# Kernel optimization log

Measured on AMD Instinct MI355X. Metric: run time of the kernel, lower is better.

Reference implementation:

```python
import jax, jax.numpy as jnp
import numpy as np

D_MODEL = 1024
D_FF = 4096
NUM_EXPERTS = 8
TOP_K = 2  # expert_capacity


def setup_inputs() -> dict:
    key = jax.random.key(0)
    ks = jax.random.split(key, 7)
    s_in = 1.0 / np.sqrt(D_MODEL)
    s_ff = 1.0 / np.sqrt(D_FF)
    x = jax.random.normal(ks[0], (2, 2048, D_MODEL), dtype=jnp.float32)
    gate_w = jax.random.uniform(ks[1], (NUM_EXPERTS, D_MODEL), jnp.float32, -s_in, s_in)
    gate_b = jax.random.uniform(ks[2], (NUM_EXPERTS,), jnp.float32, -s_in, s_in)
    w1 = jax.random.uniform(ks[3], (NUM_EXPERTS, D_MODEL, D_FF), jnp.float32, -s_in, s_in)
    b1 = jax.random.uniform(ks[4], (NUM_EXPERTS, D_FF), jnp.float32, -s_in, s_in)
    w2 = jax.random.uniform(ks[5], (NUM_EXPERTS, D_FF, D_MODEL), jnp.float32, -s_ff, s_ff)
    b2 = jax.random.uniform(ks[6], (NUM_EXPERTS, D_MODEL), jnp.float32, -s_ff, s_ff)
    return {"x": x, "gate_w": gate_w, "gate_b": gate_b,
            "w1": w1, "b1": b1, "w2": w2, "b2": b2}


def reference(x, gate_w, gate_b, w1, b1, w2, b2):
    E = gate_w.shape[0]
    # Router
    logits = jnp.einsum('bsd,ed->bse', x, gate_w) + gate_b  # [B,S,E]
    top_vals, top_idx = jax.lax.top_k(logits, TOP_K)        # [B,S,K]
    top_w = jax.nn.softmax(top_vals, axis=-1)               # softmax over the top-k logits
    probs = jax.nn.softmax(logits, axis=-1)
    usage = probs.mean(axis=(0, 1))                         # [E]
    load_balancing_loss = E * jnp.sum(usage ** 2) - 1.0
    # Combine weights: sum over top-k slots of weight * one_hot(expert)
    combine = jnp.sum(top_w[..., None] * jax.nn.one_hot(top_idx, E, dtype=x.dtype), axis=2)  # [B,S,E]
    # All experts over all tokens (faithful to the naive dense-then-mask module)
    h = jax.nn.gelu(jnp.einsum('bsd,edf->ebsf', x, w1) + b1[:, None, None, :], approximate=False)
    expert_out = jnp.einsum('ebsf,efd->ebsd', h, w2) + b2[:, None, None, :]  # [E,B,S,D]
    output = jnp.einsum('bse,ebsd->bsd', combine, expert_out)
    return output, load_balancing_loss
```

## Files before the change

### kernel.cpp

```cpp
#include <hip/hip_runtime.h>
#include <hip/hip_bf16.h>
#include <math.h>


#define D_MODEL 1024
#define D_FF    4096
#define NE      8
#define NTOK    4096
#define CAP     4096

typedef __attribute__((ext_vector_type(4))) float f32x4;
typedef __attribute__((ext_vector_type(4))) short s16x4;
typedef __attribute__((ext_vector_type(8))) short s16x8;

__device__ __forceinline__ short f2bf(float f) {
    union { float f; unsigned u; } v; v.f = f;
    unsigned r = v.u + 0x7FFFu + ((v.u >> 16) & 1u);
    return (short)(r >> 16);
}

__device__ __forceinline__ float gelu_f(float x) {
    float u = x * x;
    float v = __builtin_fmaf(0.044715f, u, 1.0f);
    float y2 = 1.5957691216057308f * x * v;
    float r = __builtin_amdgcn_rcpf(__expf(y2) + 1.0f);
    return x - x * r;
}

__device__ __forceinline__ void gload16(const void* g, void* l) {
    __builtin_amdgcn_global_load_lds(
        (const __attribute__((address_space(1))) unsigned*)g,
        (__attribute__((address_space(3))) unsigned*)l, 16, 0, 0);
}

__global__ __launch_bounds__(256) void router_kernel(
    const float* __restrict__ x, const float* __restrict__ gw,
    const float* __restrict__ gb,
    float* __restrict__ usage, int* __restrict__ eidx, float* __restrict__ wgt,
    short* __restrict__ xb)
{
    __shared__ float s_gw[NE][D_MODEL];
    __shared__ float s_usage[NE];
    int tid = threadIdx.x;
    for (int i = tid * 4; i < NE * D_MODEL; i += 256 * 4)
        *(f32x4*)&s_gw[0][i] = *(const f32x4*)(gw + i);
    if (tid < NE) s_usage[tid] = 0.f;
    __syncthreads();

    int wid = tid >> 6, lane = tid & 63;
    int wave_stride = gridDim.x * 4;
    float l_usage[NE];
#pragma unroll
    for (int e = 0; e < NE; e++) l_usage[e] = 0.f;

    for (int t = blockIdx.x * 4 + wid; t < NTOK; t += wave_stride) {
        const float* xr = x + (size_t)t * D_MODEL;
        short* xbr = xb + (size_t)t * D_MODEL;
        float acc[NE];
#pragma unroll
        for (int e = 0; e < NE; e++) acc[e] = 0.f;
        for (int i = lane * 4; i < D_MODEL; i += 64 * 4) {
            f32x4 xv = *(const f32x4*)(xr + i);
            s16x4 bv;
#pragma unroll
            for (int j = 0; j < 4; j++) bv[j] = f2bf(xv[j]);
            *(s16x4*)(xbr + i) = bv;
#pragma unroll
            for (int e = 0; e < NE; e++) {
                f32x4 gv = *(const f32x4*)&s_gw[e][i];
                acc[e] += xv[0]*gv[0] + xv[1]*gv[1] + xv[2]*gv[2] + xv[3]*gv[3];
            }
        }
#pragma unroll
        for (int e = 0; e < NE; e++) {
            float a = acc[e];
            for (int off = 32; off; off >>= 1) a += __shfl_down(a, off);
            acc[e] = a;
        }
        if (lane == 0) {
            float logits[NE];
            float mx = -1e30f;
#pragma unroll
            for (int e = 0; e < NE; e++) { logits[e] = acc[e] + gb[e]; mx = fmaxf(mx, logits[e]); }
            float se = 0.f;
            float pe[NE];
#pragma unroll
            for (int e = 0; e < NE; e++) { pe[e] = expf(logits[e] - mx); se += pe[e]; }
            float inv = 1.f / se;
#pragma unroll
            for (int e = 0; e < NE; e++) l_usage[e] += pe[e] * inv;
            int i0 = 0;
#pragma unroll
            for (int e = 1; e < NE; e++) if (logits[e] > logits[i0]) i0 = e;
            int i1 = -1;
#pragma unroll
            for (int e = 0; e < NE; e++) {
                if (e == i0) continue;
                if (i1 < 0 || logits[e] > logits[i1]) i1 = e;
            }
            float w0 = 1.f / (1.f + expf(logits[i1] - logits[i0]));
            eidx[t] = i0 | (i1 << 8);
            wgt[t] = w0;
        }
    }
    if (lane == 0) {
#pragma unroll
        for (int e = 0; e < NE; e++) atomicAdd(&s_usage[e], l_usage[e]);
    }
    __syncthreads();
    if (tid < NE) atomicAdd(&usage[tid], s_usage[tid]);
}

__global__ __launch_bounds__(256) void build_lists(
    const int* __restrict__ eidx, const float* __restrict__ wgt,
    int* __restrict__ cnt, int* __restrict__ tok_list, float* __restrict__ wt_list,
    int* __restrict__ tok2slot, float* __restrict__ wgt_p)
{
    int e = blockIdx.x;
    __shared__ int s_cnt;
    if (threadIdx.x == 0) s_cnt = 0;
    __syncthreads();
    for (int t = threadIdx.x; t < NTOK; t += 256) {
        int p = eidx[t];
        float w0 = wgt[t];
        if (e == 0) wgt_p[t] = w0;
        if ((p & 255) == e) {
            int s = atomicAdd(&s_cnt, 1);
            tok_list[e * CAP + s] = t; wt_list[e * CAP + s] = w0;
            tok2slot[2 * t] = (e << 16) | s;
        }
        if ((p >> 8) == e) {
            int s = atomicAdd(&s_cnt, 1);
            tok_list[e * CAP + s] = t; wt_list[e * CAP + s] = 1.f - w0;
            tok2slot[2 * t + 1] = (e << 16) | s;
        }
    }
    __syncthreads();
    if (threadIdx.x == 0) cnt[e] = s_cnt;
}

__global__ void compute_offsets(const int* __restrict__ cnt, int* __restrict__ offsets)
{
    int o = 0;
    for (int e = 0; e < NE; e++) { offsets[e] = o; o += cnt[e]; }
}

__global__ void write_loss(const float* __restrict__ usage, float* __restrict__ out_loss)
{
    float s = 0.f;
    for (int e = 0; e < NE; e++) { float u = usage[e] / (float)NTOK; s += u * u; }
    *out_loss = (float)NE * s - 1.f;
}

__global__ __launch_bounds__(256) void transpose_cvt(
    const float* __restrict__ src, short* __restrict__ dst, int R, int C)
{
    __shared__ float tile[64][65];
    int e = blockIdx.z;
    src += (size_t)e * R * C;
    dst += (size_t)e * R * C;
    int c0 = blockIdx.x * 64, r0 = blockIdx.y * 64;
    int tid = threadIdx.x;
    int lr = tid >> 2, lc = (tid & 3) * 16;

    const float* s = src + (size_t)(r0 + lr) * C + c0 + lc;
#pragma unroll
    for (int j = 0; j < 4; j++)
        *(f32x4*)&tile[lr][lc + j * 4] = *(const f32x4*)(s + j * 4);
    __syncthreads();

    short* d = dst + (size_t)(c0 + lr) * R + r0 + lc;
    s16x8 v0, v1;
#pragma unroll
    for (int j = 0; j < 8; j++) v0[j] = f2bf(tile[lc + j][lr]);
#pragma unroll
    for (int j = 0; j < 8; j++) v1[j] = f2bf(tile[lc + 8 + j][lr]);
    *(s16x8*)d = v0;
    *(s16x8*)(d + 8) = v1;
}

#define GEMM_STAGE(AS, BS, KT)                       \
    gload16(asrc0 + (KT), &AS[wid * 16][0]);         \
    gload16(asrc1 + (KT), &AS[64 + wid * 16][0]);    \
    gload16(bsrc0 + (KT), &BS[wid * 16][0]);         \
    gload16(bsrc1 + (KT), &BS[64 + wid * 16][0]);

#define GEMM_COMPUTE(AS, BS)                                                   \
    {                                                                          \
        s16x8 a[4], b[4];                                                      \
        int cidx = (kgr ^ ((lrow >> 1) & 3)) * 8;                              \
        _Pragma("unroll")                                                      \
        for (int i = 0; i < 4; i++) {                                          \
            a[i] = *(const s16x8*)&AS[wr * 64 + i * 16 + lrow][cidx];          \
            b[i] = *(const s16x8*)&BS[wc * 64 + i * 16 + lrow][cidx];          \
        }                                                                      \
        _Pragma("unroll")                                                      \
        for (int i = 0; i < 4; i++)                                            \
            _Pragma("unroll")                                                  \
            for (int j = 0; j < 4; j++)                                        \
                acc[i][j] = __builtin_amdgcn_mfma_f32_16x16x32_bf16(           \
                    a[i], b[j], acc[i][j], 0, 0, 0);                           \
    }

__global__ __launch_bounds__(256) void gemm1_kernel(
    const short* __restrict__ XB, const short* __restrict__ W1T,
    const float* __restrict__ b1, const int* __restrict__ cnt,
    const int* __restrict__ offsets, const int* __restrict__ tok_list,
    short* __restrict__ H)
{
    int r = blockIdx.x;
    int s = (r & 7) * 1024 + (r >> 3);
    int bx = s & 31;
    int by = s >> 5;
    int e  = by >> 5;
    int tm = by & 31;
    int ce = cnt[e];
    if (tm * 128 >= ce) return;
    int n0 = bx * 128;

    __shared__ __align__(16) short As[128][32];
    __shared__ __align__(16) short Bs[128][32];

    int tid = threadIdx.x;
    int lane = tid & 63, wid = tid >> 6;
    int wr = wid >> 1, wc = wid & 1;
    int lrow = lane & 15, kgr = lane >> 4;

    int srow = wid * 16 + (lane >> 2);
    int scol = ((lane & 3) ^ ((lane >> 3) & 3)) * 8;
    int am0 = tm * 128 + srow, am1 = am0 + 64;
    int tok0 = tok_list[e * CAP + (am0 < ce ? am0 : 0)];
    int tok1 = tok_list[e * CAP + (am1 < ce ? am1 : 0)];
    const short* asrc0 = XB + (size_t)tok0 * D_MODEL + scol;
    const short* asrc1 = XB + (size_t)tok1 * D_MODEL + scol;
    const short* bsrc0 = W1T + ((size_t)e * D_FF + n0 + srow) * D_MODEL + scol;
    const short* bsrc1 = bsrc0 + (size_t)64 * D_MODEL;

    f32x4 acc[4][4] = {};
    for (int kt = 0; kt < D_MODEL; kt += 32) {
        GEMM_STAGE(As, Bs, kt);
        __syncthreads();
        GEMM_COMPUTE(As, Bs);
        __syncthreads();
    }

    int offe = offsets[e];
    float bn[4];
#pragma unroll
    for (int j = 0; j < 4; j++) bn[j] = b1[e * D_FF + n0 + wc * 64 + j * 16 + lrow];
#pragma unroll
    for (int i = 0; i < 4; i++) {
#pragma unroll
        for (int q = 0; q < 4; q++) {
            int m = tm * 128 + wr * 64 + i * 16 + kgr * 4 + q;
            if (m >= ce) continue;
            short* hrow = H + (size_t)(offe + m) * D_FF;
#pragma unroll
            for (int j = 0; j < 4; j++) {
                int n = n0 + wc * 64 + j * 16 + lrow;
                hrow[n] = f2bf(gelu_f(acc[i][j][q] + bn[j]));
            }
        }
    }
}

__global__ __launch_bounds__(256) void gemm2_y_kernel(
    const short* __restrict__ H, const short* __restrict__ W2T,
    const float* __restrict__ b2, const int* __restrict__ cnt,
    const int* __restrict__ offsets, float* __restrict__ Y)
{
    int r = blockIdx.x;
    int s = (r & 7) * 256 + (r >> 3);
    int bx = s & 7;
    int by = s >> 3;
    int e  = by >> 5;
    int tm = by & 31;
    int ce = cnt[e];
    if (tm * 128 >= ce) return;
    int offe = offsets[e];
    int n0 = bx * 128;

    __shared__ __align__(16) short As[128][32];
    __shared__ __align__(16) short Bs[128][32];

    int tid = threadIdx.x;
    int lane = tid & 63, wid = tid >> 6;
    int wr = wid >> 1, wc = wid & 1;
    int lrow = lane & 15, kgr = lane >> 4;

    int srow = wid * 16 + (lane >> 2);
    int scol = ((lane & 3) ^ ((lane >> 3) & 3)) * 8;
    int am0 = tm * 128 + srow, am1 = am0 + 64;
    const short* asrc0 = H + (size_t)(offe + (am0 < ce ? am0 : 0)) * D_FF + scol;
    const short* asrc1 = H + (size_t)(offe + (am1 < ce ? am1 : 0)) * D_FF + scol;
    const short* bsrc0 = W2T + ((size_t)e * D_MODEL + n0 + srow) * D_FF + scol;
    const short* bsrc1 = bsrc0 + (size_t)64 * D_FF;

    f32x4 acc[4][4] = {};
    for (int kt = 0; kt < D_FF; kt += 32) {
        GEMM_STAGE(As, Bs, kt);
        __syncthreads();
        GEMM_COMPUTE(As, Bs);
        __syncthreads();
    }

    float bn[4];
#pragma unroll
    for (int j = 0; j < 4; j++) bn[j] = b2[e * D_MODEL + n0 + wc * 64 + j * 16 + lrow];
#pragma unroll
    for (int i = 0; i < 4; i++) {
#pragma unroll
        for (int q = 0; q < 4; q++) {
            int m = tm * 128 + wr * 64 + i * 16 + kgr * 4 + q;
            if (m >= ce) continue;
            float* yrow = Y + (size_t)(offe + m) * D_MODEL;
#pragma unroll
            for (int j = 0; j < 4; j++) {
                int n = n0 + wc * 64 + j * 16 + lrow;
                yrow[n] = acc[i][j][q] + bn[j];
            }
        }
    }
}

__global__ __launch_bounds__(256) void combine_kernel(
    const float* __restrict__ Y, const int* __restrict__ tok2slot,
    const float* __restrict__ wgt_p, const int* __restrict__ offsets,
    float* __restrict__ out)
{
    int t = blockIdx.x;
    int d = threadIdx.x * 4;
    int p0 = tok2slot[2 * t], p1 = tok2slot[2 * t + 1];
    int s0 = offsets[p0 >> 16] + (p0 & 0xFFFF);
    int s1 = offsets[p1 >> 16] + (p1 & 0xFFFF);
    float w0 = wgt_p[t], w1 = 1.f - w0;
    f32x4 a = *(const f32x4*)(Y + (size_t)s0 * D_MODEL + d);
    f32x4 b = *(const f32x4*)(Y + (size_t)s1 * D_MODEL + d);
    f32x4 r;
#pragma unroll
    for (int j = 0; j < 4; j++) r[j] = w0 * a[j] + w1 * b[j];
    *(f32x4*)(out + (size_t)t * D_MODEL + d) = r;
}

__global__ __launch_bounds__(256) void gemm2_kernel(
    const short* __restrict__ H, const short* __restrict__ W2T,
    const float* __restrict__ b2, const int* __restrict__ cnt,
    const int* __restrict__ offsets, const int* __restrict__ tok_list,
    const float* __restrict__ wt_list, float* __restrict__ out)
{
    int e  = blockIdx.y >> 5;
    int tm = blockIdx.y & 31;
    int ce = cnt[e];
    if (tm * 128 >= ce) return;
    int offe = offsets[e];
    int n0 = blockIdx.x * 128;
    int kz = blockIdx.z;
    const int KSPAN = D_FF / 2;
    int kbase = kz * KSPAN;

    __shared__ __align__(16) short As[128][32];
    __shared__ __align__(16) short Bs[128][32];

    int tid = threadIdx.x;
    int lane = tid & 63, wid = tid >> 6;
    int wr = wid >> 1, wc = wid & 1;
    int lrow = lane & 15, kgr = lane >> 4;

    int srow = wid * 16 + (lane >> 2);
    int scol = ((lane & 3) ^ ((lane >> 3) & 3)) * 8;
    int am0 = tm * 128 + srow, am1 = am0 + 64;
    const short* asrc0 = H + (size_t)(offe + (am0 < ce ? am0 : 0)) * D_FF + kbase + scol;
    const short* asrc1 = H + (size_t)(offe + (am1 < ce ? am1 : 0)) * D_FF + kbase + scol;
    const short* bsrc0 = W2T + ((size_t)e * D_MODEL + n0 + srow) * D_FF + kbase + scol;
    const short* bsrc1 = bsrc0 + (size_t)64 * D_FF;

    f32x4 acc[4][4] = {};
    for (int kt = 0; kt < KSPAN; kt += 32) {
        GEMM_STAGE(As, Bs, kt);
        __syncthreads();
        GEMM_COMPUTE(As, Bs);
        __syncthreads();
    }

    float bn[4];
#pragma unroll
    for (int j = 0; j < 4; j++)
        bn[j] = (kz == 0) ? b2[e * D_MODEL + n0 + wc * 64 + j * 16 + lrow] : 0.f;
#pragma unroll
    for (int i = 0; i < 4; i++) {
#pragma unroll
        for (int q = 0; q < 4; q++) {
            int m = tm * 128 + wr * 64 + i * 16 + kgr * 4 + q;
            if (m >= ce) continue;
            int tokm = tok_list[e * CAP + m];
            float wt = wt_list[e * CAP + m];
            float* orow = out + (size_t)tokm * D_MODEL;
#pragma unroll
            for (int j = 0; j < 4; j++) {
                int n = n0 + wc * 64 + j * 16 + lrow;
                atomicAdd(&orow[n], wt * (acc[i][j][q] + bn[j]));
            }
        }
    }
}

extern "C" void kernel_launch(void* const* d_in, const int* in_sizes, int n_in,
                              void* d_out, int out_size, void* d_ws, size_t ws_size,
                              hipStream_t stream)
{
    const float* x  = (const float*)d_in[0];
    const float* gw = (const float*)d_in[1];
    const float* gb = (const float*)d_in[2];
    const float* w1 = (const float*)d_in[3];
    const float* b1 = (const float*)d_in[4];
    const float* w2 = (const float*)d_in[5];
    const float* b2 = (const float*)d_in[6];
    float* out = (float*)d_out;

    char* w = (char*)d_ws;
    int*   cnt      = (int*)(w + 0);
    float* usage    = (float*)(w + 32);
    int*   offsets  = (int*)(w + 64);
    int*   tok_list = (int*)(w + 128);
    float* wt_list  = (float*)(w + 128 + 131072);
    int*   tok2slot = (int*)(w + 128 + 262144);
    float* wgt_p    = (float*)(w + 128 + 262144 + 32768);
    short* WT       = (short*)(w + 311424);
    short* H        = (short*)(w + 311424 + 67108864ull);
    float* Y        = (float*)(w + 311424 + 2ull * 67108864ull);
    size_t need_y   = 311424 + 2ull * 67108864ull + 33554432ull;
    bool   use_y    = ws_size >= need_y;
    int*   eidx     = (int*)WT;
    float* wgt      = (float*)(WT + NTOK * 2);
    short* XB       = (short*)d_out;

    hipMemsetAsync(d_ws, 0, 128, stream);

    router_kernel<<<256, 256, 0, stream>>>(x, gw, gb, usage, eidx, wgt, XB);
    build_lists<<<NE, 256, 0, stream>>>(eidx, wgt, cnt, tok_list, wt_list, tok2slot, wgt_p);
    compute_offsets<<<1, 1, 0, stream>>>(cnt, offsets);

    transpose_cvt<<<dim3(D_FF / 64, D_MODEL / 64, NE), 256, 0, stream>>>(w1, WT, D_MODEL, D_FF);
    gemm1_kernel<<<(D_FF / 128) * NE * (CAP / 128), 256, 0, stream>>>(
        XB, WT, b1, cnt, offsets, tok_list, H);

    transpose_cvt<<<dim3(D_MODEL / 64, D_FF / 64, NE), 256, 0, stream>>>(w2, WT, D_FF, D_MODEL);

    if (use_y) {
        write_loss<<<1, 1, 0, stream>>>(usage, out + (size_t)NTOK * D_MODEL);
        gemm2_y_kernel<<<2048, 256, 0, stream>>>(H, WT, b2, cnt, offsets, Y);
        combine_kernel<<<NTOK, 256, 0, stream>>>(Y, tok2slot, wgt_p, offsets, out);
    } else {
        hipMemsetAsync(d_out, 0, (size_t)out_size * sizeof(float), stream);
        write_loss<<<1, 1, 0, stream>>>(usage, out + (size_t)NTOK * D_MODEL);
        gemm2_kernel<<<dim3(D_MODEL / 128, NE * (CAP / 128), 2), 256, 0, stream>>>(
            H, WT, b2, cnt, offsets, tok_list, wt_list, out);
    }
}
```

Baseline: 348.1 us.

## Merge router and both weight transposes into one prep kernel; fold offsets/loss into build_lists

When the workspace is large enough, the router and the bf16 transposes of w1 and w2 now run as block ranges of one kernel, with separate W1T and W2T buffers. This removes several launches and lets the weight conversions overlap with routing. build_lists also computes offsets and the loss in its last block, found through an atomic counter, which drops two tiny serial launches. In exchange it needs an extra 64MB of workspace, and the prep kernel's shared-memory union is sized for the router, which can lower occupancy for the transpose blocks.

```diff
diff --git a/kernel.cpp b/kernel.cpp
--- a/kernel.cpp
+++ b/kernel.cpp
@@ -33,27 +33,28 @@
         (__attribute__((address_space(3))) unsigned*)l, 16, 0, 0);
 }
 
-__global__ __launch_bounds__(256) void router_kernel(
+
+struct RouterSmem { float gw[NE][D_MODEL]; float us[NE]; };
+
+__device__ void router_body(
     const float* __restrict__ x, const float* __restrict__ gw,
-    const float* __restrict__ gb,
-    float* __restrict__ usage, int* __restrict__ eidx, float* __restrict__ wgt,
-    short* __restrict__ xb)
-{
-    __shared__ float s_gw[NE][D_MODEL];
-    __shared__ float s_usage[NE];
+    const float* __restrict__ gb, float* __restrict__ usage,
+    int* __restrict__ eidx, float* __restrict__ wgt, short* __restrict__ xb,
+    RouterSmem* sm, int rb, int nblk)
+{
     int tid = threadIdx.x;
     for (int i = tid * 4; i < NE * D_MODEL; i += 256 * 4)
-        *(f32x4*)&s_gw[0][i] = *(const f32x4*)(gw + i);
-    if (tid < NE) s_usage[tid] = 0.f;
+        *(f32x4*)&sm->gw[0][i] = *(const f32x4*)(gw + i);
+    if (tid < NE) sm->us[tid] = 0.f;
     __syncthreads();
 
     int wid = tid >> 6, lane = tid & 63;
-    int wave_stride = gridDim.x * 4;
+    int wave_stride = nblk * 4;
     float l_usage[NE];
 #pragma unroll
     for (int e = 0; e < NE; e++) l_usage[e] = 0.f;
 
-    for (int t = blockIdx.x * 4 + wid; t < NTOK; t += wave_stride) {
+    for (int t = rb * 4 + wid; t < NTOK; t += wave_stride) {
         const float* xr = x + (size_t)t * D_MODEL;
         short* xbr = xb + (size_t)t * D_MODEL;
         float acc[NE];
@@ -67,7 +68,7 @@
             *(s16x4*)(xbr + i) = bv;
 #pragma unroll
             for (int e = 0; e < NE; e++) {
-                f32x4 gv = *(const f32x4*)&s_gw[e][i];
+                f32x4 gv = *(const f32x4*)&sm->gw[e][i];
                 acc[e] += xv[0]*gv[0] + xv[1]*gv[1] + xv[2]*gv[2] + xv[3]*gv[3];
             }
         }
@@ -105,16 +106,80 @@
     }
     if (lane == 0) {
 #pragma unroll
-        for (int e = 0; e < NE; e++) atomicAdd(&s_usage[e], l_usage[e]);
+        for (int e = 0; e < NE; e++) atomicAdd(&sm->us[e], l_usage[e]);
     }
     __syncthreads();
-    if (tid < NE) atomicAdd(&usage[tid], s_usage[tid]);
+    if (tid < NE) atomicAdd(&usage[tid], sm->us[tid]);
+}
+
+__device__ void transpose_body(
+    const float* __restrict__ src, short* __restrict__ dst, int R, int C,
+    int bx, int by, int e, float (*tile)[65])
+{
+    src += (size_t)e * R * C;
+    dst += (size_t)e * R * C;
+    int c0 = bx * 64, r0 = by * 64;
+    int tid = threadIdx.x;
+    int lr = tid >> 2, lc = (tid & 3) * 16;
+
+    const float* s = src + (size_t)(r0 + lr) * C + c0 + lc;
+#pragma unroll
+    for (int j = 0; j < 4; j++)
+        *(f32x4*)&tile[lr][lc + j * 4] = *(const f32x4*)(s + j * 4);
+    __syncthreads();
+
+    short* d = dst + (size_t)(c0 + lr) * R + r0 + lc;
+    s16x8 v0, v1;
+#pragma unroll
+    for (int j = 0; j < 8; j++) v0[j] = f2bf(tile[lc + j][lr]);
+#pragma unroll
+    for (int j = 0; j < 8; j++) v1[j] = f2bf(tile[lc + 8 + j][lr]);
+    *(s16x8*)d = v0;
+    *(s16x8*)(d + 8) = v1;
+}
+
+__global__ __launch_bounds__(256) void prep_kernel(
+    const float* __restrict__ x, const float* __restrict__ gw,
+    const float* __restrict__ gb, float* __restrict__ usage,
+    int* __restrict__ eidx, float* __restrict__ wgt, short* __restrict__ xb,
+    const float* __restrict__ w1, short* __restrict__ w1t,
+    const float* __restrict__ w2, short* __restrict__ w2t)
+{
+    __shared__ union { RouterSmem r; float tile[64][65]; } sm;
+    int b = blockIdx.x;
+    if (b < 256) {
+        router_body(x, gw, gb, usage, eidx, wgt, xb, &sm.r, b, 256);
+    } else if (b < 256 + 8192) {
+        int q = b - 256;
+        transpose_body(w1, w1t, D_MODEL, D_FF, q & 63, (q >> 6) & 15, q >> 10, sm.tile);
+    } else {
+        int q = b - 256 - 8192;
+        transpose_body(w2, w2t, D_FF, D_MODEL, q & 15, (q >> 4) & 63, q >> 10, sm.tile);
+    }
+}
+
+__global__ __launch_bounds__(256) void router_kernel(
+    const float* __restrict__ x, const float* __restrict__ gw,
+    const float* __restrict__ gb, float* __restrict__ usage,
+    int* __restrict__ eidx, float* __restrict__ wgt, short* __restrict__ xb)
+{
+    __shared__ RouterSmem sm;
+    router_body(x, gw, gb, usage, eidx, wgt, xb, &sm, blockIdx.x, gridDim.x);
+}
+
+__global__ __launch_bounds__(256) void transpose_cvt(
+    const float* __restrict__ src, short* __restrict__ dst, int R, int C)
+{
+    __shared__ float tile[64][65];
+    transpose_body(src, dst, R, C, blockIdx.x, blockIdx.y, blockIdx.z, tile);
 }
 
 __global__ __launch_bounds__(256) void build_lists(
     const int* __restrict__ eidx, const float* __restrict__ wgt,
     int* __restrict__ cnt, int* __restrict__ tok_list, float* __restrict__ wt_list,
-    int* __restrict__ tok2slot, float* __restrict__ wgt_p)
+    int* __restrict__ tok2slot, float* __restrict__ wgt_p,
+    int* __restrict__ done, int* __restrict__ offsets,
+    const float* __restrict__ usage, float* __restrict__ out_loss)
 {
     int e = blockIdx.x;
     __shared__ int s_cnt;
@@ -136,13 +201,20 @@
         }
     }
     __syncthreads();
-    if (threadIdx.x == 0) cnt[e] = s_cnt;
-}
-
-__global__ void compute_offsets(const int* __restrict__ cnt, int* __restrict__ offsets)
-{
-    int o = 0;
-    for (int e = 0; e < NE; e++) { offsets[e] = o; o += cnt[e]; }
+    if (threadIdx.x == 0) {
+        cnt[e] = s_cnt;
+        __threadfence();
+        if (atomicAdd(done, 1) == NE - 1) {
+            __threadfence();
+            int o = 0;
+            for (int k = 0; k < NE; k++) { offsets[k] = o; o += cnt[k]; }
+            if (out_loss) {
+                float s = 0.f;
+                for (int k = 0; k < NE; k++) { float u = usage[k] / (float)NTOK; s += u * u; }
+                *out_loss = (float)NE * s - 1.f;
+            }
+        }
+    }
 }
 
 __global__ void write_loss(const float* __restrict__ usage, float* __restrict__ out_loss)
@@ -150,33 +222,6 @@
     float s = 0.f;
     for (int e = 0; e < NE; e++) { float u = usage[e] / (float)NTOK; s += u * u; }
     *out_loss = (float)NE * s - 1.f;
-}
-
-__global__ __launch_bounds__(256) void transpose_cvt(
-    const float* __restrict__ src, short* __restrict__ dst, int R, int C)
-{
-    __shared__ float tile[64][65];
-    int e = blockIdx.z;
-    src += (size_t)e * R * C;
-    dst += (size_t)e * R * C;
-    int c0 = blockIdx.x * 64, r0 = blockIdx.y * 64;
-    int tid = threadIdx.x;
-    int lr = tid >> 2, lc = (tid & 3) * 16;
-
-    const float* s = src + (size_t)(r0 + lr) * C + c0 + lc;
-#pragma unroll
-    for (int j = 0; j < 4; j++)
-        *(f32x4*)&tile[lr][lc + j * 4] = *(const f32x4*)(s + j * 4);
-    __syncthreads();
-
-    short* d = dst + (size_t)(c0 + lr) * R + r0 + lc;
-    s16x8 v0, v1;
-#pragma unroll
-    for (int j = 0; j < 8; j++) v0[j] = f2bf(tile[lc + j][lr]);
-#pragma unroll
-    for (int j = 0; j < 8; j++) v1[j] = f2bf(tile[lc + 8 + j][lr]);
-    *(s16x8*)d = v0;
-    *(s16x8*)(d + 8) = v1;
 }
 
 #define GEMM_STAGE(AS, BS, KT)                       \
@@ -421,38 +466,63 @@
     int*   cnt      = (int*)(w + 0);
     float* usage    = (float*)(w + 32);
     int*   offsets  = (int*)(w + 64);
+    int*   done     = (int*)(w + 96);
     int*   tok_list = (int*)(w + 128);
     float* wt_list  = (float*)(w + 128 + 131072);
     int*   tok2slot = (int*)(w + 128 + 262144);
     float* wgt_p    = (float*)(w + 128 + 262144 + 32768);
-    short* WT       = (short*)(w + 311424);
-    short* H        = (short*)(w + 311424 + 67108864ull);
-    float* Y        = (float*)(w + 311424 + 2ull * 67108864ull);
-    size_t need_y   = 311424 + 2ull * 67108864ull + 33554432ull;
-    bool   use_y    = ws_size >= need_y;
-    int*   eidx     = (int*)WT;
-    float* wgt      = (float*)(WT + NTOK * 2);
+    const size_t MB64 = 67108864ull;
     short* XB       = (short*)d_out;
-
+    float* out_loss = out + (size_t)NTOK * D_MODEL;
+
+    size_t need_sep = 311424 + 3ull * MB64;
+    size_t need_y1  = 311424 + 2ull * MB64 + 33554432ull;
     hipMemsetAsync(d_ws, 0, 128, stream);
 
+    if (ws_size >= need_sep) {
+        short* W1T = (short*)(w + 311424);
+        short* W2T = (short*)(w + 311424 + MB64);
+        short* H   = (short*)(w + 311424 + 2 * MB64);
+        float* Y   = (float*)W1T;
+        int*   eidx = (int*)H;
+        float* wgt  = (float*)((char*)H + 16384);
+
+        prep_kernel<<<256 + 8192 + 8192, 256, 0, stream>>>(
+            x, gw, gb, usage, eidx, wgt, XB, w1, W1T, w2, W2T);
+        build_lists<<<NE, 256, 0, stream>>>(
+            eidx, wgt, cnt, tok_list, wt_list, tok2slot, wgt_p,
+            done, offsets, usage, out_loss);
+        gemm1_kernel<<<(D_FF / 128) * NE * (CAP / 128), 256, 0, stream>>>(
+            XB, W1T, b1, cnt, offsets, tok_list, H);
+        gemm2_y_kernel<<<2048, 256, 0, stream>>>(H, W2T, b2, cnt, offsets, Y);
+        combine_kernel<<<NTOK, 256, 0, stream>>>(Y, tok2slot, wgt_p, offsets, out);
+        return;
+    }
+
+    short* WT  = (short*)(w + 311424);
+    short* H   = (short*)(w + 311424 + MB64);
+    float* Y   = (float*)(w + 311424 + 2 * MB64);
+    bool   use_y = ws_size >= need_y1;
+    int*   eidx = (int*)WT;
+    float* wgt  = (float*)(WT + NTOK * 2);
+
     router_kernel<<<256, 256, 0, stream>>>(x, gw, gb, usage, eidx, wgt, XB);
-    build_lists<<<NE, 256, 0, stream>>>(eidx, wgt, cnt, tok_list, wt_list, tok2slot, wgt_p);
-    compute_offsets<<<1, 1, 0, stream>>>(cnt, offsets);
+    build_lists<<<NE, 256, 0, stream>>>(
+        eidx, wgt, cnt, tok_list, wt_list, tok2slot, wgt_p,
+        done, offsets, usage, nullptr);
 
     transpose_cvt<<<dim3(D_FF / 64, D_MODEL / 64, NE), 256, 0, stream>>>(w1, WT, D_MODEL, D_FF);
     gemm1_kernel<<<(D_FF / 128) * NE * (CAP / 128), 256, 0, stream>>>(
         XB, WT, b1, cnt, offsets, tok_list, H);
-
     transpose_cvt<<<dim3(D_MODEL / 64, D_FF / 64, NE), 256, 0, stream>>>(w2, WT, D_FF, D_MODEL);
 
     if (use_y) {
-        write_loss<<<1, 1, 0, stream>>>(usage, out + (size_t)NTOK * D_MODEL);
+        write_loss<<<1, 1, 0, stream>>>(usage, out_loss);
         gemm2_y_kernel<<<2048, 256, 0, stream>>>(H, WT, b2, cnt, offsets, Y);
         combine_kernel<<<NTOK, 256, 0, stream>>>(Y, tok2slot, wgt_p, offsets, out);
     } else {
         hipMemsetAsync(d_out, 0, (size_t)out_size * sizeof(float), stream);
-        write_loss<<<1, 1, 0, stream>>>(usage, out + (size_t)NTOK * D_MODEL);
+        write_loss<<<1, 1, 0, stream>>>(usage, out_loss);
         gemm2_kernel<<<dim3(D_MODEL / 128, NE * (CAP / 128), 2), 256, 0, stream>>>(
             H, WT, b2, cnt, offsets, tok_list, wt_list, out);
     }
```

After: 316.0 us, median of 3. 9.2% less time.
